# Performance work log

Hardware: AMD Instinct MI355X
Metric: run time of the kernel (lower is better)

## Reference

```python
import jax, jax.numpy as jnp
import numpy as np

B = 8192
D_IN = 512
D_HID = 256
D_OUT = 128
EPS_STD = 1e-5
EPS_NORM = 1e-12


def _embed(x, W1, b1, W2, b2):
    # head: Linear -> ReLU -> Linear
    h = jax.nn.relu(x @ W1 + b1)          # (b, 256)
    y = h @ W2 + b2                        # (b, 128)
    # white(): per-feature batch whitening (center + unit std, unbiased like torch.std)
    mu = jnp.mean(y, axis=0, keepdims=True)
    sd = jnp.std(y, axis=0, keepdims=True, ddof=1) + EPS_STD
    y = (y - mu) / sd
    # F.normalize(p=2, dim=1)
    n = jnp.maximum(jnp.linalg.norm(y, axis=1, keepdims=True), EPS_NORM)
    return y / n


def _pair_loss(v1, v2):
    b = v1.shape[0]
    cat = jnp.concatenate([v1, v2], axis=0)            # (2b, d)
    inner = v1 @ cat.T                                  # (b, 2b) == broadcasted (v1*cat).sum(2)
    mask = jnp.concatenate(
        [1.0 - jnp.eye(b, dtype=inner.dtype), jnp.ones((b, b), dtype=inner.dtype)], axis=1)
    logits = inner * mask                               # zero out self-similarity logits
    logp = jax.nn.log_softmax(logits, axis=1)
    tgt = jnp.arange(b, 2 * b)                          # positive = matching row in v2 block
    return -jnp.take_along_axis(logp, tgt[:, None], axis=1).mean()


def setup_inputs() -> dict:
    key = jax.random.key(0)
    ks = jax.random.split(key, 16)
    def lin_init(k, fin, fout):
        bound = 1.0 / np.sqrt(fin)
        kw, kb = jax.random.split(k)
        W = jax.random.uniform(kw, (fin, fout), jnp.float32, -bound, bound)
        b = jax.random.uniform(kb, (fout,), jnp.float32, -bound, bound)
        return W, b
    inp = {
        'x_B': jax.random.normal(ks[0], (B, D_IN), jnp.float32),
        'x_E': jax.random.normal(ks[1], (B, D_IN), jnp.float32),
        'x_F': jax.random.normal(ks[2], (B, D_IN), jnp.float32),
    }
    for i, m in enumerate('BEF'):
        W1, b1 = lin_init(ks[3 + 2 * i], D_IN, D_HID)
        W2, b2 = lin_init(ks[4 + 2 * i], D_HID, D_OUT)
        inp[f'W1_{m}'] = W1; inp[f'b1_{m}'] = b1
        inp[f'W2_{m}'] = W2; inp[f'b2_{m}'] = b2
    return inp


def reference(x_B, x_E, x_F,
              W1_B, b1_B, W2_B, b2_B,
              W1_E, b1_E, W2_E, b2_E,
              W1_F, b1_F, W2_F, b2_F):
    zB = _embed(x_B, W1_B, b1_B, W2_B, b2_B)
    zE = _embed(x_E, W1_E, b1_E, W2_E, b2_E)
    zF = _embed(x_F, W1_F, b1_F, W2_F, b2_F)
    pairs = [(zB, zE), (zB, zF), (zE, zF)]  # itertools.combinations order
    loss = sum(_pair_loss(v1, v2) for v1, v2 in pairs) / len(pairs)
    return loss
```

## Files before the change

kernel.cpp:

```cpp
#include <hip/hip_runtime.h>
#include <hip/hip_bf16.h>
#include <math.h>

#define NROWS 8192
#define DIN   512
#define DHID  256
#define DOUT  128
#define LOG2E 1.4426950408889634f

typedef unsigned short ushort_t;
typedef __attribute__((ext_vector_type(8))) short bf16x8;
typedef __attribute__((ext_vector_type(4))) float f32x4;

#if defined(__has_builtin)
#  if __has_builtin(__builtin_amdgcn_exp2f)
#    define FAST_EXP2(x) __builtin_amdgcn_exp2f(x)
#  else
#    define FAST_EXP2(x) exp2f(x)
#  endif
#else
#  define FAST_EXP2(x) exp2f(x)
#endif

__device__ __forceinline__ short f2bf(float x) {
  __hip_bfloat16 h = __float2bfloat16(x);
  return *(short*)&h;
}

__device__ __forceinline__ float bf2f(ushort_t v) {
  unsigned int u = ((unsigned int)v) << 16;
  union { unsigned int u; float f; } c; c.u = u;
  return c.f;
}

__device__ __forceinline__ bf16x8 cvt8(float4 lo, float4 hi) {
  bf16x8 r;
  r[0] = f2bf(lo.x); r[1] = f2bf(lo.y); r[2] = f2bf(lo.z); r[3] = f2bf(lo.w);
  r[4] = f2bf(hi.x); r[5] = f2bf(hi.y); r[6] = f2bf(hi.z); r[7] = f2bf(hi.w);
  return r;
}

__device__ __forceinline__ void dma16(const void* g, void* l) {
  __builtin_amdgcn_global_load_lds(
      (const __attribute__((address_space(1))) unsigned int*)g,
      (__attribute__((address_space(3))) unsigned int*)l, 16, 0, 0);
}

__global__ __launch_bounds__(256) void prep_w_kernel(
    const float* __restrict__ W1_0, const float* __restrict__ W1_1,
    const float* __restrict__ W1_2,
    const float* __restrict__ W2_0, const float* __restrict__ W2_1,
    const float* __restrict__ W2_2,
    ushort_t* __restrict__ w1t3, ushort_t* __restrict__ w2t3,
    float* __restrict__ zero_region, float* __restrict__ out)
{
  const int z = blockIdx.z, gx = blockIdx.x, gy = blockIdx.y;
  const int tid = threadIdx.x;
  if (z == 0) {
    int b = gy * 4 + gx;
#pragma unroll
    for (int j = 0; j < 4; j++) {
      int idx = b * 256 + tid + j * 12288;
      if (idx < 41792) zero_region[idx] = 0.0f;
    }
    if (b == 0 && tid == 0) out[0] = 0.0f;
  }
  const float* W1 = z == 0 ? W1_0 : (z == 1 ? W1_1 : W1_2);
  const float* W2 = z == 0 ? W2_0 : (z == 1 ? W2_1 : W2_2);

  __shared__ float t[64][65];
  if (gy < 8) {
    const int k0 = gy * 64, n0 = gx * 64;
#pragma unroll
    for (int it = 0; it < 16; it++) {
      int r = it * 4 + (tid >> 6), c = tid & 63;
      t[r][c] = W1[(size_t)(k0 + r) * DHID + n0 + c];
    }
    __syncthreads();
    ushort_t* dst = w1t3 + (size_t)z * DHID * DIN;
#pragma unroll
    for (int it = 0; it < 16; it++) {
      int n = it * 4 + (tid >> 6), k = tid & 63;
      dst[(size_t)(n0 + n) * DIN + k0 + k] = (ushort_t)f2bf(t[k][n]);
    }
  } else {
    if (gx >= 2) return;
    const int k0 = (gy - 8) * 64, n0 = gx * 64;
#pragma unroll
    for (int it = 0; it < 16; it++) {
      int r = it * 4 + (tid >> 6), c = tid & 63;
      t[r][c] = W2[(size_t)(k0 + r) * DOUT + n0 + c];
    }
    __syncthreads();
    ushort_t* dst = w2t3 + (size_t)z * DOUT * DHID;
#pragma unroll
    for (int it = 0; it < 16; it++) {
      int n = it * 4 + (tid >> 6), k = tid & 63;
      dst[(size_t)(n0 + n) * DHID + k0 + k] = (ushort_t)f2bf(t[k][n]);
    }
  }
}

#define MLP_BUF 24576
__global__ __launch_bounds__(256, 2) void mlp_kernel(
    const float* __restrict__ x0, const float* __restrict__ x1,
    const float* __restrict__ x2,
    const ushort_t* __restrict__ w1t3,
    const float* __restrict__ b1_0, const float* __restrict__ b1_1,
    const float* __restrict__ b1_2,
    const ushort_t* __restrict__ w2t3,
    const float* __restrict__ b2_0, const float* __restrict__ b2_1,
    const float* __restrict__ b2_2,
    ushort_t* __restrict__ y3,
    float* __restrict__ colsum, float* __restrict__ colsumsq)
{
  const int z = blockIdx.y;
  const float* X  = z == 0 ? x0 : (z == 1 ? x1 : x2);
  const float* B1 = z == 0 ? b1_0 : (z == 1 ? b1_1 : b1_2);
  const float* B2 = z == 0 ? b2_0 : (z == 1 ? b2_1 : b2_2);
  const ushort_t* W1t = w1t3 + (size_t)z * DHID * DIN;
  const ushort_t* W2t = w2t3 + (size_t)z * DOUT * DHID;
  ushort_t* Y = y3 + (size_t)z * NROWS * DOUT;
  float* csum = colsum + z * DOUT;
  float* csq  = colsumsq + z * DOUT;

  __shared__ __align__(16) char lds[2 * MLP_BUF];
  ushort_t* hs = (ushort_t*)lds;

  const int tid = threadIdx.x, lane = tid & 63, wave = tid >> 6;
  const int quad = lane >> 4, l16 = lane & 15;
  const int m0 = blockIdx.x * 64;

  const char* w1b = (const char*)W1t;
  const char* wsrc[4];
#pragma unroll
  for (int jj = 0; jj < 4; jj++)
    wsrc[jj] = w1b + (size_t)(16 * (wave * 4 + jj) + l16) * 1024 + quad * 16;
  const int row8 = lane >> 3, slot = lane & 7;
  const int gseg = (slot + row8) & 7;
  const char* xsrc[2];
#pragma unroll
  for (int jj = 0; jj < 2; jj++)
    xsrc[jj] = (const char*)X +
        (size_t)(m0 + 8 * (wave * 2 + jj) + row8) * 2048 + gseg * 16;

  f32x4 acc1[4][4] = {};
#pragma unroll
  for (int jj = 0; jj < 4; jj++)
    dma16(wsrc[jj], lds + (wave * 4 + jj) * 1024);
#pragma unroll
  for (int jj = 0; jj < 2; jj++)
    dma16(xsrc[jj], lds + 16384 + (wave * 2 + jj) * 1024);
  __syncthreads();

  for (int c = 0; c < 16; c++) {
    const int buf = c & 1;
    if (c + 1 < 16) {
      char* dst = lds + (buf ^ 1) * MLP_BUF;
#pragma unroll
      for (int jj = 0; jj < 4; jj++)
        dma16(wsrc[jj] + (c + 1) * 64, dst + (wave * 4 + jj) * 1024);
#pragma unroll
      for (int jj = 0; jj < 2; jj++)
        dma16(xsrc[jj] + (c + 1) * 128, dst + 16384 + (wave * 2 + jj) * 1024);
    }
    const char* wb = lds + buf * MLP_BUF;
    const char* xb = wb + 16384;
    bf16x8 a[4];
#pragma unroll
    for (int mt = 0; mt < 4; mt++) {
      const int r = mt * 16 + l16, r7 = r & 7;
      const int s0 = (2 * quad - r7) & 7, s1 = (2 * quad + 1 - r7) & 7;
      float4 v0 = *(const float4*)(xb + r * 128 + s0 * 16);
      float4 v1 = *(const float4*)(xb + r * 128 + s1 * 16);
      a[mt] = cvt8(v0, v1);
    }
    bf16x8 b[4];
#pragma unroll
    for (int ct = 0; ct < 4; ct++)
      b[ct] = *(const bf16x8*)(wb + (wave * 4 + ct) * 1024 + quad * 256 +
                               l16 * 16);
#pragma unroll
    for (int mt = 0; mt < 4; mt++)
#pragma unroll
      for (int ct = 0; ct < 4; ct++)
        acc1[mt][ct] = __builtin_amdgcn_mfma_f32_16x16x32_bf16(
            a[mt], b[ct], acc1[mt][ct], 0, 0, 0);
    __syncthreads();
  }

  bf16x8 b2f[2][8];
#pragma unroll
  for (int ct = 0; ct < 2; ct++)
#pragma unroll
    for (int kk = 0; kk < 8; kk++)
      b2f[ct][kk] = *(const bf16x8*)(W2t +
          (size_t)(wave * 32 + ct * 16 + l16) * DHID + kk * 32 + quad * 8);

#pragma unroll
  for (int ct = 0; ct < 4; ct++) {
    float bb = B1[wave * 64 + ct * 16 + l16];
#pragma unroll
    for (int mt = 0; mt < 4; mt++)
#pragma unroll
      for (int reg = 0; reg < 4; reg++) {
        float v = fmaxf(acc1[mt][ct][reg] + bb, 0.0f);
        hs[(mt * 16 + quad * 4 + reg) * 264 + wave * 64 + ct * 16 + l16] =
            (ushort_t)f2bf(v);
      }
  }
  __syncthreads();

  f32x4 acc2[4][2] = {};
#pragma unroll
  for (int kk = 0; kk < 8; kk++) {
    bf16x8 a2[4];
#pragma unroll
    for (int mt = 0; mt < 4; mt++)
      a2[mt] = *(const bf16x8*)(hs + (mt * 16 + l16) * 264 + kk * 32 +
                                quad * 8);
#pragma unroll
    for (int mt = 0; mt < 4; mt++)
#pragma unroll
      for (int ct = 0; ct < 2; ct++)
        acc2[mt][ct] = __builtin_amdgcn_mfma_f32_16x16x32_bf16(
            a2[mt], b2f[ct][kk], acc2[mt][ct], 0, 0, 0);
  }

#pragma unroll
  for (int ct = 0; ct < 2; ct++) {
    const int colo = wave * 32 + ct * 16 + l16;
    float bb = B2[colo];
    float cs = 0.0f, cq = 0.0f;
#pragma unroll
    for (int mt = 0; mt < 4; mt++)
#pragma unroll
      for (int reg = 0; reg < 4; reg++) {
        float v = acc2[mt][ct][reg] + bb;
        Y[(size_t)(m0 + mt * 16 + quad * 4 + reg) * DOUT + colo] =
            (ushort_t)f2bf(v);
        cs += v; cq += v * v;
      }
    cs += __shfl_xor(cs, 16, 64); cs += __shfl_xor(cs, 32, 64);
    cq += __shfl_xor(cq, 16, 64); cq += __shfl_xor(cq, 32, 64);
    if (lane < 16) {
      atomicAdd(&csum[colo], cs);
      atomicAdd(&csq[colo], cq);
    }
  }
}

__global__ __launch_bounds__(256) void whiten_kernel(
    const ushort_t* __restrict__ y3,
    const float* __restrict__ colsum, const float* __restrict__ colsumsq,
    ushort_t* __restrict__ zB, ushort_t* __restrict__ zE,
    ushort_t* __restrict__ zF,
    ushort_t* __restrict__ zBs, ushort_t* __restrict__ zEs,
    float* __restrict__ pos)
{
  const int tid = threadIdx.x, lane = tid & 63, wave = tid >> 6;
  const int row = blockIdx.x * 4 + wave;
  const size_t base = (size_t)row * DOUT;
  const size_t hsz = (size_t)NROWS * DOUT;
  const int c0 = lane, c1 = lane + 64;

  float mu[3][2], isd[3][2];
#pragma unroll
  for (int h = 0; h < 3; h++) {
#pragma unroll
    for (int cc = 0; cc < 2; cc++) {
      const int idx = h * DOUT + (cc ? c1 : c0);
      float m = colsum[idx] * (1.0f / NROWS);
      float var = (colsumsq[idx] - (float)NROWS * m * m) *
                  (1.0f / (NROWS - 1));
      mu[h][cc] = m;
      isd[h][cc] = 1.0f / (sqrtf(fmaxf(var, 0.0f)) + 1e-5f);
    }
  }

  float vB0 = (bf2f(y3[base + c0])           - mu[0][0]) * isd[0][0];
  float vB1 = (bf2f(y3[base + c1])           - mu[0][1]) * isd[0][1];
  float vE0 = (bf2f(y3[base + hsz + c0])     - mu[1][0]) * isd[1][0];
  float vE1 = (bf2f(y3[base + hsz + c1])     - mu[1][1]) * isd[1][1];
  float vF0 = (bf2f(y3[base + 2 * hsz + c0]) - mu[2][0]) * isd[2][0];
  float vF1 = (bf2f(y3[base + 2 * hsz + c1]) - mu[2][1]) * isd[2][1];

  float nB = vB0 * vB0 + vB1 * vB1;
  float nE = vE0 * vE0 + vE1 * vE1;
  float nF = vF0 * vF0 + vF1 * vF1;
#pragma unroll
  for (int o = 1; o < 64; o <<= 1) {
    nB += __shfl_xor(nB, o, 64);
    nE += __shfl_xor(nE, o, 64);
    nF += __shfl_xor(nF, o, 64);
  }
  float iB = 1.0f / fmaxf(sqrtf(nB), 1e-12f);
  float iE = 1.0f / fmaxf(sqrtf(nE), 1e-12f);
  float iF = 1.0f / fmaxf(sqrtf(nF), 1e-12f);
  float zb0 = vB0 * iB, zb1 = vB1 * iB;
  float ze0 = vE0 * iE, ze1 = vE1 * iE;
  float zf0 = vF0 * iF, zf1 = vF1 * iF;

  zB[base + c0]  = (ushort_t)f2bf(zb0);
  zB[base + c1]  = (ushort_t)f2bf(zb1);
  zE[base + c0]  = (ushort_t)f2bf(ze0);
  zE[base + c1]  = (ushort_t)f2bf(ze1);
  zF[base + c0]  = (ushort_t)f2bf(zf0);
  zF[base + c1]  = (ushort_t)f2bf(zf1);
  zBs[base + c0] = (ushort_t)f2bf(zb0 * LOG2E);
  zBs[base + c1] = (ushort_t)f2bf(zb1 * LOG2E);
  zEs[base + c0] = (ushort_t)f2bf(ze0 * LOG2E);
  zEs[base + c1] = (ushort_t)f2bf(ze1 * LOG2E);

  float pBE = zb0 * ze0 + zb1 * ze1;
  float pBF = zb0 * zf0 + zb1 * zf1;
  float pEF = ze0 * zf0 + ze1 * zf1;
#pragma unroll
  for (int o = 1; o < 64; o <<= 1) {
    pBE += __shfl_xor(pBE, o, 64);
    pBF += __shfl_xor(pBF, o, 64);
    pEF += __shfl_xor(pEF, o, 64);
  }
  if (lane == 0) {
    pos[row]             = pBE;
    pos[NROWS + row]     = pBF;
    pos[2 * NROWS + row] = pEF;
  }
}

#define NBLK_GRAM 1824
__global__ __launch_bounds__(256, 3) void gram_kernel(
    const ushort_t* __restrict__ zB, const ushort_t* __restrict__ zE,
    const ushort_t* __restrict__ zF,
    const ushort_t* __restrict__ zBs, const ushort_t* __restrict__ zEs,
    float* __restrict__ rowsum, const float* __restrict__ pos,
    unsigned int* __restrict__ counter, float* __restrict__ out)
{
  const int id = blockIdx.x;
  int combo, mblk, cbase, nch, do_col;
  if (id < 768) {
    combo = 2 + (id >> 8);
    const int r = id & 255;
    mblk = r >> 3; cbase = (r & 7) * 1024; nch = 32; do_col = 0;
  } else {
    const int sid = id - 768;
    combo = sid / 528;
    int t = sid - combo * 528;
    int p = 0, acc0 = 0;
    while (acc0 + (32 - p) <= t) { acc0 += 32 - p; p++; }
    const int q = p + (t - acc0);
    mblk = p; cbase = q << 8; nch = 8; do_col = (q > p);
  }

  const ushort_t *U, *V;
  float* rs;
  switch (combo) {
    case 0:  U = zBs; V = zB; rs = rowsum;             break;
    case 1:  U = zEs; V = zE; rs = rowsum + NROWS;     break;
    case 2:  U = zBs; V = zE; rs = rowsum + 2 * NROWS; break;
    case 3:  U = zBs; V = zF; rs = rowsum + 3 * NROWS; break;
    default: U = zEs; V = zF; rs = rowsum + 4 * NROWS; break;
  }

  const int tid = threadIdx.x, lane = tid & 63, wave = tid >> 6;
  const int quad = lane >> 4, l16 = lane & 15;
  const int m0 = mblk * 256 + wave * 64;

  __shared__ __align__(16) ushort_t sbuf[2][4096];

  const ushort_t* ua = U + (size_t)(m0 + l16) * DOUT + quad * 8;
  bf16x8 a[4][4];
#pragma unroll
  for (int rt = 0; rt < 4; rt++)
#pragma unroll
    for (int ki = 0; ki < 4; ki++)
      a[rt][ki] = *(const bf16x8*)(ua + rt * 16 * DOUT + ki * 32);

  const char* Vb = (const char*)V;
  const int r_ = lane & 31, hi_ = lane >> 5;
  const int s0 = 4 * wave + hi_, s1 = 4 * wave + 2 + hi_;
  const char* g0 = Vb + (size_t)(cbase + r_) * 256 + s0 * 16;
  const char* g1 = Vb + (size_t)(cbase + r_) * 256 + s1 * 16;

  float rsum[4][4] = {};
  const f32x4 zero = {0.0f, 0.0f, 0.0f, 0.0f};

  dma16(g0, &sbuf[0][(2 * wave) * 512]);
  dma16(g1, &sbuf[0][(2 * wave + 1) * 512]);
  __syncthreads();

  for (int c = 0; c < nch; c++) {
    const int buf = c & 1;
    if (c + 1 < nch) {
      const size_t go = (size_t)(c + 1) * 8192;
      dma16(g0 + go, &sbuf[buf ^ 1][(2 * wave) * 512]);
      dma16(g1 + go, &sbuf[buf ^ 1][(2 * wave + 1) * 512]);
    }
    const char* sb = (const char*)&sbuf[buf][0];
    bf16x8 b[4][2];
#pragma unroll
    for (int ki = 0; ki < 4; ki++)
#pragma unroll
      for (int ct = 0; ct < 2; ct++)
        b[ki][ct] = *(const bf16x8*)(sb + (ki * 4 + quad) * 512 +
                                     (ct * 16 + l16) * 16);
    f32x4 acc[4][2];
#pragma unroll
    for (int ki = 0; ki < 4; ki++)
#pragma unroll
      for (int rt = 0; rt < 4; rt++)
#pragma unroll
        for (int ct = 0; ct < 2; ct++)
          acc[rt][ct] = __builtin_amdgcn_mfma_f32_16x16x32_bf16(
              a[rt][ki], b[ki][ct], ki == 0 ? zero : acc[rt][ct], 0, 0, 0);
    float csum0 = 0.0f, csum1 = 0.0f;
#pragma unroll
    for (int rt = 0; rt < 4; rt++)
#pragma unroll
      for (int reg = 0; reg < 4; reg++) {
        float e0 = FAST_EXP2(acc[rt][0][reg]);
        float e1 = FAST_EXP2(acc[rt][1][reg]);
        rsum[rt][reg] += e0 + e1;
        csum0 += e0; csum1 += e1;
      }
    if (do_col) {
      csum0 += __shfl_xor(csum0, 16, 64); csum0 += __shfl_xor(csum0, 32, 64);
      csum1 += __shfl_xor(csum1, 16, 64); csum1 += __shfl_xor(csum1, 32, 64);
      if (quad == 0) {
        const int colc = cbase + c * 32;
        atomicAdd(&rs[colc + l16], csum0);
        atomicAdd(&rs[colc + 16 + l16], csum1);
      }
    }
    __syncthreads();
  }

#pragma unroll
  for (int rt = 0; rt < 4; rt++)
#pragma unroll
    for (int reg = 0; reg < 4; reg++) {
      float s = rsum[rt][reg];
      s += __shfl_xor(s, 1, 64);
      s += __shfl_xor(s, 2, 64);
      s += __shfl_xor(s, 4, 64);
      s += __shfl_xor(s, 8, 64);
      if (l16 == 0)
        atomicAdd(&rs[m0 + rt * 16 + quad * 4 + reg], s);
    }

  __shared__ int is_last;
  __syncthreads();
  if (tid == 0) {
    __threadfence();
    unsigned int old = atomicAdd(counter, 1u);
    is_last = (old == (unsigned int)(NBLK_GRAM - 1)) ? 1 : 0;
  }
  __syncthreads();
  if (is_last) {
    __threadfence();
    const float corr = 1.0f - expf(1.0f);
    float local = 0.0f;
    for (int i = tid; i < NROWS; i += 256) {
      float sB = __hip_atomic_load(&rowsum[i], __ATOMIC_RELAXED,
                                   __HIP_MEMORY_SCOPE_AGENT) + corr;
      float sE = __hip_atomic_load(&rowsum[NROWS + i], __ATOMIC_RELAXED,
                                   __HIP_MEMORY_SCOPE_AGENT) + corr;
      float cBE = __hip_atomic_load(&rowsum[2 * NROWS + i], __ATOMIC_RELAXED,
                                    __HIP_MEMORY_SCOPE_AGENT);
      float cBF = __hip_atomic_load(&rowsum[3 * NROWS + i], __ATOMIC_RELAXED,
                                    __HIP_MEMORY_SCOPE_AGENT);
      float cEF = __hip_atomic_load(&rowsum[4 * NROWS + i], __ATOMIC_RELAXED,
                                    __HIP_MEMORY_SCOPE_AGENT);
      local += __logf(sB + cBE) - pos[i];
      local += __logf(sB + cBF) - pos[NROWS + i];
      local += __logf(sE + cEF) - pos[2 * NROWS + i];
    }
    __shared__ float red[4];
#pragma unroll
    for (int o = 32; o > 0; o >>= 1) local += __shfl_down(local, o, 64);
    if (lane == 0) red[wave] = local;
    __syncthreads();
    if (tid == 0)
      out[0] = (red[0] + red[1] + red[2] + red[3]) *
               (1.0f / (3.0f * (float)NROWS));
  }
}

extern "C" void kernel_launch(void* const* d_in, const int* in_sizes, int n_in,
                              void* d_out, int out_size, void* d_ws, size_t ws_size,
                              hipStream_t stream)
{
  const float* xs[3] = {(const float*)d_in[0], (const float*)d_in[1], (const float*)d_in[2]};
  const float* W1[3] = {(const float*)d_in[3], (const float*)d_in[7],  (const float*)d_in[11]};
  const float* b1[3] = {(const float*)d_in[4], (const float*)d_in[8],  (const float*)d_in[12]};
  const float* W2[3] = {(const float*)d_in[5], (const float*)d_in[9],  (const float*)d_in[13]};
  const float* b2[3] = {(const float*)d_in[6], (const float*)d_in[10], (const float*)d_in[14]};

  float* ws = (float*)d_ws;
  float* colsum   = ws;
  float* colsumsq = ws + 384;
  float* rowsum   = ws + 768;
  unsigned int* counter = (unsigned int*)(ws + 41728);
  float* pos      = ws + 42496;
  ushort_t* w1t3 = (ushort_t*)(ws + 67072);
  ushort_t* w2t3 = (ushort_t*)(ws + 263680);
  ushort_t* y3b  = (ushort_t*)(ws + 312832);
  ushort_t* zB   = (ushort_t*)(ws + 1885696);
  ushort_t* zE   = zB  + (size_t)NROWS * DOUT;
  ushort_t* zF   = zE  + (size_t)NROWS * DOUT;
  ushort_t* zBs  = zF  + (size_t)NROWS * DOUT;
  ushort_t* zEs  = zBs + (size_t)NROWS * DOUT;

  prep_w_kernel<<<dim3(4, 12, 3), 256, 0, stream>>>(
      W1[0], W1[1], W1[2], W2[0], W2[1], W2[2], w1t3, w2t3, ws, (float*)d_out);
  mlp_kernel<<<dim3(128, 3), 256, 0, stream>>>(
      xs[0], xs[1], xs[2], w1t3, b1[0], b1[1], b1[2],
      w2t3, b2[0], b2[1], b2[2], y3b, colsum, colsumsq);
  whiten_kernel<<<2048, 256, 0, stream>>>(
      y3b, colsum, colsumsq, zB, zE, zF, zBs, zEs, pos);
  gram_kernel<<<NBLK_GRAM, 256, 0, stream>>>(
      zB, zE, zF, zBs, zEs, rowsum, pos, counter, (float*)d_out);
}
```

Measured before the change: 265.2 us.

## Replace triangular symmetric Gram tiling with a uniform full 3D grid

Removes the symmetry trick for the two self-similarity combos, which computed only upper-triangular 256x256 tiles and added column sums through atomics. Every combo now computes full 256x1024 row tiles from a uniform dim3(32,8,5) grid with 32 chunks each. This drops the per-chunk column reductions and atomics and the irregular block-index mapping, but does roughly a quarter more MFMA and exp work on the self-combos.

```diff
diff --git a/kernel.cpp b/kernel.cpp
--- a/kernel.cpp
+++ b/kernel.cpp
@@ -328,7 +328,9 @@
   }
 }
 
-#define NBLK_GRAM 1824
+#define G_CH  32
+#define G_NCH 32
+#define NBLK_GRAM 1280
 __global__ __launch_bounds__(256, 3) void gram_kernel(
     const ushort_t* __restrict__ zB, const ushort_t* __restrict__ zE,
     const ushort_t* __restrict__ zF,
@@ -336,25 +338,9 @@
     float* __restrict__ rowsum, const float* __restrict__ pos,
     unsigned int* __restrict__ counter, float* __restrict__ out)
 {
-  const int id = blockIdx.x;
-  int combo, mblk, cbase, nch, do_col;
-  if (id < 768) {
-    combo = 2 + (id >> 8);
-    const int r = id & 255;
-    mblk = r >> 3; cbase = (r & 7) * 1024; nch = 32; do_col = 0;
-  } else {
-    const int sid = id - 768;
-    combo = sid / 528;
-    int t = sid - combo * 528;
-    int p = 0, acc0 = 0;
-    while (acc0 + (32 - p) <= t) { acc0 += 32 - p; p++; }
-    const int q = p + (t - acc0);
-    mblk = p; cbase = q << 8; nch = 8; do_col = (q > p);
-  }
-
   const ushort_t *U, *V;
   float* rs;
-  switch (combo) {
+  switch (blockIdx.z) {
     case 0:  U = zBs; V = zB; rs = rowsum;             break;
     case 1:  U = zEs; V = zE; rs = rowsum + NROWS;     break;
     case 2:  U = zBs; V = zE; rs = rowsum + 2 * NROWS; break;
@@ -364,7 +350,8 @@
 
   const int tid = threadIdx.x, lane = tid & 63, wave = tid >> 6;
   const int quad = lane >> 4, l16 = lane & 15;
-  const int m0 = mblk * 256 + wave * 64;
+  const int m0 = blockIdx.x * 256 + wave * 64;
+  const int col0 = blockIdx.y * (G_CH * G_NCH);
 
   __shared__ __align__(16) ushort_t sbuf[2][4096];
 
@@ -379,8 +366,8 @@
   const char* Vb = (const char*)V;
   const int r_ = lane & 31, hi_ = lane >> 5;
   const int s0 = 4 * wave + hi_, s1 = 4 * wave + 2 + hi_;
-  const char* g0 = Vb + (size_t)(cbase + r_) * 256 + s0 * 16;
-  const char* g1 = Vb + (size_t)(cbase + r_) * 256 + s1 * 16;
+  const char* g0 = Vb + (size_t)(col0 + r_) * 256 + s0 * 16;
+  const char* g1 = Vb + (size_t)(col0 + r_) * 256 + s1 * 16;
 
   float rsum[4][4] = {};
   const f32x4 zero = {0.0f, 0.0f, 0.0f, 0.0f};
@@ -389,9 +376,9 @@
   dma16(g1, &sbuf[0][(2 * wave + 1) * 512]);
   __syncthreads();
 
-  for (int c = 0; c < nch; c++) {
+  for (int c = 0; c < G_NCH; c++) {
     const int buf = c & 1;
-    if (c + 1 < nch) {
+    if (c + 1 < G_NCH) {
       const size_t go = (size_t)(c + 1) * 8192;
       dma16(g0 + go, &sbuf[buf ^ 1][(2 * wave) * 512]);
       dma16(g1 + go, &sbuf[buf ^ 1][(2 * wave + 1) * 512]);
@@ -413,25 +400,11 @@
         for (int ct = 0; ct < 2; ct++)
           acc[rt][ct] = __builtin_amdgcn_mfma_f32_16x16x32_bf16(
               a[rt][ki], b[ki][ct], ki == 0 ? zero : acc[rt][ct], 0, 0, 0);
-    float csum0 = 0.0f, csum1 = 0.0f;
 #pragma unroll
     for (int rt = 0; rt < 4; rt++)
 #pragma unroll
-      for (int reg = 0; reg < 4; reg++) {
-        float e0 = FAST_EXP2(acc[rt][0][reg]);
-        float e1 = FAST_EXP2(acc[rt][1][reg]);
-        rsum[rt][reg] += e0 + e1;
-        csum0 += e0; csum1 += e1;
-      }
-    if (do_col) {
-      csum0 += __shfl_xor(csum0, 16, 64); csum0 += __shfl_xor(csum0, 32, 64);
-      csum1 += __shfl_xor(csum1, 16, 64); csum1 += __shfl_xor(csum1, 32, 64);
-      if (quad == 0) {
-        const int colc = cbase + c * 32;
-        atomicAdd(&rs[colc + l16], csum0);
-        atomicAdd(&rs[colc + 16 + l16], csum1);
-      }
-    }
+      for (int reg = 0; reg < 4; reg++)
+        rsum[rt][reg] += FAST_EXP2(acc[rt][0][reg]) + FAST_EXP2(acc[rt][1][reg]);
     __syncthreads();
   }
 
@@ -518,6 +491,6 @@
       w2t3, b2[0], b2[1], b2[2], y3b, colsum, colsumsq);
   whiten_kernel<<<2048, 256, 0, stream>>>(
       y3b, colsum, colsumsq, zB, zE, zF, zBs, zEs, pos);
-  gram_kernel<<<NBLK_GRAM, 256, 0, stream>>>(
+  gram_kernel<<<dim3(32, 8, 5), 256, 0, stream>>>(
       zB, zE, zF, zBs, zEs, rowsum, pos, counter, (float*)d_out);
 }
```

Measured after the change: 264.6 us. No clear change (-0.2%).
